# Kernel optimization log

Measured on AMD Instinct MI355X. Metric: run time of the kernel, lower is better.

Reference implementation:

```python
import jax, jax.numpy as jnp
import numpy as np

N, E, ND, D = 100000, 200000, 128, 32


def linear_bn(x, W, g, b, eps=1e-5):
    # Linear (no bias) followed by BatchNorm1d in training mode (batch stats)
    y = x @ W
    mu = jnp.mean(y, axis=0)
    var = jnp.var(y, axis=0)
    return g * (y - mu) * jax.lax.rsqrt(var + eps) + b


def setup_inputs() -> dict:
    key = jax.random.key(0)
    ks = jax.random.split(key, 16)
    s = 0.05
    return {
        "node": jax.random.normal(ks[0], (N, ND), jnp.float32),
        "edge_index": jax.random.randint(ks[1], (E, 2), 0, N, jnp.int64),
        "edge": jax.random.normal(ks[2], (E, D), jnp.float32),
        "hidden": jax.random.normal(ks[3], (1, E, D), jnp.float32),
        "W1": jax.random.normal(ks[4], (2 * ND, 256), jnp.float32) * s,
        "g1": jnp.ones((256,), jnp.float32), "b1": jnp.zeros((256,), jnp.float32),
        "W2": jax.random.normal(ks[5], (256, 256), jnp.float32) * s,
        "g2": jnp.ones((256,), jnp.float32), "b2": jnp.zeros((256,), jnp.float32),
        "W3": jax.random.normal(ks[6], (256, 128), jnp.float32) * s,
        "g3": jnp.ones((128,), jnp.float32), "b3": jnp.zeros((128,), jnp.float32),
        "W4": jax.random.normal(ks[7], (128, D * D), jnp.float32) * s,
        "g4": jnp.ones((D * D,), jnp.float32), "b4": jnp.zeros((D * D,), jnp.float32),
        "bias": jax.random.uniform(ks[8], (D,), jnp.float32, -1.0 / np.sqrt(D), 1.0 / np.sqrt(D)),
        "W_ih": jax.random.normal(ks[9], (3 * D, D), jnp.float32) * s,
        "W_hh": jax.random.normal(ks[10], (3 * D, D), jnp.float32) * s,
        "b_ih": jnp.zeros((3 * D,), jnp.float32),
        "b_hh": jnp.zeros((3 * D,), jnp.float32),
    }


def reference(node, edge_index, edge, hidden, W1, g1, b1, W2, g2, b2, W3, g3, b3,
              W4, g4, b4, bias, W_ih, W_hh, b_ih, b_hh):
    num_edge, edge_dim = edge.shape
    # gather endpoint node features and concat -> [E, 2*node_dim]
    x_ij = jnp.concatenate([node[edge_index[:, 0]], node[edge_index[:, 1]]], axis=1)
    h = jax.nn.relu(linear_bn(x_ij, W1, g1, b1))
    h = jax.nn.relu(linear_bn(h, W2, g2, b2))
    h = jax.nn.relu(linear_bn(h, W3, g3, b3))
    A = linear_bn(h, W4, g4, b4).reshape(num_edge, edge_dim, edge_dim)
    # per-edge small matmul: [E,1,D] @ [E,D,D] -> [E,D]
    message = jnp.einsum('ed,edf->ef', edge, A)
    message = jax.nn.relu(message + bias)
    # single-step GRU (seq_len=1, edges as batch)
    h0 = hidden[0]
    gi = message @ W_ih.T + b_ih
    gh = h0 @ W_hh.T + b_hh
    i_r, i_z, i_n = jnp.split(gi, 3, axis=1)
    h_r, h_z, h_n = jnp.split(gh, 3, axis=1)
    r = jax.nn.sigmoid(i_r + h_r)
    z = jax.nn.sigmoid(i_z + h_z)
    n = jnp.tanh(i_n + r * h_n)
    h_new = (1.0 - z) * n + z * h0
    return h_new, h_new[None]
```

## Files before the change

kernel.cpp:

```cpp
#include <hip/hip_runtime.h>
#include <hip/hip_fp16.h>

#define NE 200000
#define NT 6250
#define NT64 3125
#define GRAM_BLOCKS 512

__device__ float g_st[21248];
__device__ unsigned short g_c4h[1024];
__device__ int g_flag64;

#define SUM1 (&g_st[0])
#define SQ1  (&g_st[256])
#define SUM2 (&g_st[512])
#define SQ2  (&g_st[768])
#define SUM3 (&g_st[1024])
#define SQ3  (&g_st[1152])
#define GMAT (&g_st[1280])
#define CS3  (&g_st[17664])
#define A1   (&g_st[17792])
#define C1   (&g_st[18048])
#define A2   (&g_st[18304])
#define C2   (&g_st[18560])
#define A3   (&g_st[18816])
#define C3   (&g_st[18944])
#define A4   (&g_st[19072])
#define C4   (&g_st[20096])

typedef unsigned short u16;
typedef _Float16 f16x8 __attribute__((ext_vector_type(8)));
typedef float f32x4 __attribute__((ext_vector_type(4)));

__device__ __forceinline__ f32x4 mfma16(f16x8 a, f16x8 b, f32x4 c) {
  return __builtin_amdgcn_mfma_f32_16x16x32_f16(a, b, c, 0, 0, 0);
}
__device__ __forceinline__ u16 f2h(float x) {
  __half h = __float2half_rn(x);
  return *reinterpret_cast<u16*>(&h);
}
__device__ __forceinline__ float h2f(u16 s) {
  __half h = *reinterpret_cast<__half*>(&s);
  return __half2float(h);
}
__device__ __forceinline__ float relu_np(float t) { return (t < 0.f) ? 0.f : t; }
__device__ __forceinline__ unsigned packh2(float a, float b) {
  return (unsigned)f2h(a) | ((unsigned)f2h(b) << 16);
}

__global__ void GraphConv2_16518444221042_kernel(float* __restrict__ out,
                                                 float v, int n) {
  int i = blockIdx.x * 256 + threadIdx.x;
  if (i < n) out[i] = v;
}

__global__ void k_init(const int* __restrict__ e) {
  int i = blockIdx.x * 256 + threadIdx.x;
  if (i < 17792) g_st[i] = 0.f;
  if (i == 0) {
    int allz = 1;
    for (int k = 1; k < 128; k += 2) allz &= (e[k] == 0);
    g_flag64 = allz;
  }
}

__global__ void k_packA(const float* __restrict__ W1,
                        const float* __restrict__ W2,
                        const float* __restrict__ W3,
                        u16* __restrict__ dst) {
  int i = blockIdx.x * 256 + threadIdx.x;
  if (i >= 163840) return;
  float v;
  if (i < 65536) {
    int n = i >> 8, k = i & 255;
    v = W1[k * 256 + n];
  } else if (i < 131072) {
    int i2 = i - 65536, n = i2 >> 8, k = i2 & 255;
    v = W2[k * 256 + n];
  } else {
    int i2 = i - 131072, n = i2 >> 8, k = i2 & 255;
    v = W3[k * 128 + n];
  }
  dst[i] = f2h(v);
}

__global__ void k_packB(const float* __restrict__ W4,
                        const float* __restrict__ Wih,
                        const float* __restrict__ Whh,
                        u16* __restrict__ dst) {
  int i = blockIdx.x * 256 + threadIdx.x;
  if (i >= 137216) return;
  float v;
  if (i < 131072) {
    int n = i >> 7, k = i & 127;
    v = W4[(size_t)k * 1024 + n];
  } else if (i < 134144) {
    v = Wih[i - 131072];
  } else {
    v = Whh[i - 134144];
  }
  dst[i] = f2h(v);
}

__global__ void k_finalize(const float* __restrict__ g,
                           const float* __restrict__ b, int which, int C) {
  int j = threadIdx.x;
  if (j < C) {
    const float* sum = (which == 1) ? SUM1 : (which == 2) ? SUM2 : SUM3;
    const float* sq  = (which == 1) ? SQ1 : (which == 2) ? SQ2 : SQ3;
    float* aa = (which == 1) ? A1 : (which == 2) ? A2 : A3;
    float* cc = (which == 1) ? C1 : (which == 2) ? C2 : C3;
    const float invE = 1.f / (float)NE;
    float mu = sum[j] * invE;
    float var = fmaf(-mu, mu, sq[j] * invE);
    float s = rsqrtf(var + 1e-5f);
    float av = g[j] * s;
    aa[j] = av;
    cc[j] = fmaf(-av, mu, b[j]);
  }
}

__global__ __launch_bounds__(64) void k_finalize4(
    const float* __restrict__ W4, const float* __restrict__ g4,
    const float* __restrict__ b4) {
  __shared__ float wsh[128];
  const int lane = threadIdx.x;
  const float invE = 1.f / (float)NE;
  for (int j = blockIdx.x; j < 1024; j += gridDim.x) {
    float w0 = W4[lane * 1024 + j];
    float w1 = W4[(lane + 64) * 1024 + j];
    wsh[lane] = w0;
    wsh[lane + 64] = w1;
    __syncthreads();
    float s0 = 0.f, s1 = 0.f;
#pragma unroll 8
    for (int k = 0; k < 128; ++k) {
      float wk = wsh[k];
      s0 = fmaf(GMAT[lane * 128 + k], wk, s0);
      s1 = fmaf(GMAT[(lane + 64) * 128 + k], wk, s1);
    }
    float acc = w0 * s0 + w1 * s1;
    float mac = CS3[lane] * w0 + CS3[lane + 64] * w1;
#pragma unroll
    for (int off = 32; off > 0; off >>= 1) {
      acc += __shfl_down(acc, off);
      mac += __shfl_down(mac, off);
    }
    if (lane == 0) {
      float mu = mac * invE;
      float var = fmaf(-mu, mu, acc * invE);
      float s = rsqrtf(var + 1e-5f);
      float av = g4[j] * s;
      A4[j] = av;
      float cv = fmaf(-av, mu, b4[j]);
      C4[j] = cv;
      g_c4h[(j & 31) * 32 + (j >> 5)] = f2h(cv);
    }
    __syncthreads();
  }
}

template <int L>
__global__ __launch_bounds__(512) void k_gemmP(
    const float* __restrict__ node, const int* __restrict__ eidx,
    const u16* __restrict__ Yin, const u16* __restrict__ Wt,
    u16* __restrict__ Yout) {
  constexpr int CN = (L == 3) ? 128 : 256;
  constexpr int CTW = CN / 128;
  constexpr int LDH = 264;
  __shared__ __align__(16) u16 H[64 * LDH];
  __shared__ float csum_s[CN], csq_s[CN];
  __shared__ int idx_s[128];
  const int tid = threadIdx.x;
  float* SUMo = (L == 1) ? SUM1 : (L == 2) ? SUM2 : SUM3;
  float* SQo  = (L == 1) ? SQ1 : (L == 2) ? SQ2 : SQ3;
  const float* Ain = (L == 2) ? A1 : A2;
  const float* Cin = (L == 2) ? C1 : C2;

  const int l = tid & 63, w = tid >> 6;
  const int lr = l & 15, lg = l >> 4;

  f16x8 bfr[CTW][8];
#pragma unroll
  for (int c = 0; c < CTW; ++c)
#pragma unroll
    for (int kb = 0; kb < 8; ++kb)
      bfr[c][kb] = *(const f16x8*)&Wt[(size_t)((w * CTW + c) * 16 + lr) * 256 +
                                      kb * 32 + lg * 8];

  if (tid < CN) { csum_s[tid] = 0.f; csq_s[tid] = 0.f; }
  float sreg[CTW] = {}, qreg[CTW] = {};

  for (int t = blockIdx.x; t < NT64; t += gridDim.x) {
    const int r0 = t * 64;
    __syncthreads();
    if constexpr (L == 1) {
      if (tid < 128) {
        const int is64 = g_flag64;
        int m = tid & 63, sel = tid >> 6;
        int j = (r0 + m) * 2 + sel;
        int v = is64 ? eidx[j * 2] : eidx[j];
        v = v < 0 ? 0 : (v > 99999 ? 99999 : v);
        idx_s[sel * 64 + m] = v;
      }
      __syncthreads();
#pragma unroll
      for (int i = 0; i < 8; ++i) {
        int idx = tid + i * 512;
        int row = idx >> 6, col = (idx & 63) * 4;
        int sel = col >> 7, kc = col & 127;
        float4 v =
            *(const float4*)&node[(size_t)idx_s[sel * 64 + row] * 128 + kc];
        uint2 pk;
        pk.x = packh2(v.x, v.y);
        pk.y = packh2(v.z, v.w);
        *(uint2*)&H[row * LDH + col] = pk;
      }
    } else {
#pragma unroll
      for (int i = 0; i < 4; ++i) {
        int idx = tid + i * 512;
        int row = idx >> 5, col = (idx & 31) * 8;
        uint4 ld = *(const uint4*)&Yin[(size_t)(r0 + row) * 256 + col];
        const u16* sp = (const u16*)&ld;
        uint4 o;
        unsigned po[4];
#pragma unroll
        for (int p = 0; p < 4; ++p) {
          float v0 = relu_np(fmaf(Ain[col + 2 * p], h2f(sp[2 * p]),
                                  Cin[col + 2 * p]));
          float v1 = relu_np(fmaf(Ain[col + 2 * p + 1], h2f(sp[2 * p + 1]),
                                  Cin[col + 2 * p + 1]));
          po[p] = packh2(v0, v1);
        }
        o.x = po[0]; o.y = po[1]; o.z = po[2]; o.w = po[3];
        *(uint4*)&H[row * LDH + col] = o;
      }
    }
    __syncthreads();

    f32x4 acc[4][CTW] = {};
#pragma unroll
    for (int kb = 0; kb < 8; ++kb) {
      f16x8 a[4];
#pragma unroll
      for (int rt = 0; rt < 4; ++rt)
        a[rt] = *(const f16x8*)&H[(rt * 16 + lr) * LDH + kb * 32 + lg * 8];
#pragma unroll
      for (int c = 0; c < CTW; ++c)
#pragma unroll
        for (int rt = 0; rt < 4; ++rt)
          acc[rt][c] = mfma16(a[rt], bfr[c][kb], acc[rt][c]);
    }

#pragma unroll
    for (int c = 0; c < CTW; ++c) {
      const int col = (w * CTW + c) * 16 + lr;
#pragma unroll
      for (int rt = 0; rt < 4; ++rt)
#pragma unroll
        for (int r = 0; r < 4; ++r) {
          float v = acc[rt][c][r];
          sreg[c] += v;
          qreg[c] = fmaf(v, v, qreg[c]);
          int row = rt * 16 + lg * 4 + r;
          Yout[(size_t)(r0 + row) * CN + col] = f2h(v);
        }
    }
  }

  __syncthreads();
#pragma unroll
  for (int c = 0; c < CTW; ++c) {
    const int col = (w * CTW + c) * 16 + lr;
    atomicAdd(&csum_s[col], sreg[c]);
    atomicAdd(&csq_s[col], qreg[c]);
  }
  __syncthreads();
  if (tid < CN) {
    atomicAdd(&SUMo[tid], csum_s[tid]);
    atomicAdd(&SQo[tid], csq_s[tid]);
  }
}

__global__ __launch_bounds__(256, 2) void k_gram_m(const u16* __restrict__ y3g,
                                                   float* __restrict__ pg) {
  __shared__ u16 h3T[128 * 40];
  __shared__ float cred[128];
  const int tid = threadIdx.x;
  const int l = tid & 63, w = tid >> 6;
  const int lr = l & 15, lg = l >> 4;
  const int c4 = (tid & 31) * 4;
  const int rb = tid >> 5;
  f32x4 acc[2][8] = {};
  float csc[4] = {0.f, 0.f, 0.f, 0.f};

  for (int t = blockIdx.x; t < NT; t += gridDim.x) {
    const size_t r0 = (size_t)t * 32;
    __syncthreads();
#pragma unroll
    for (int i = 0; i < 4; ++i) {
      int row = rb + i * 8;
      ushort4 v = *(const ushort4*)&y3g[(r0 + row) * 128 + c4];
      float h[4];
      h[0] = relu_np(fmaf(A3[c4 + 0], h2f(v.x), C3[c4 + 0]));
      h[1] = relu_np(fmaf(A3[c4 + 1], h2f(v.y), C3[c4 + 1]));
      h[2] = relu_np(fmaf(A3[c4 + 2], h2f(v.z), C3[c4 + 2]));
      h[3] = relu_np(fmaf(A3[c4 + 3], h2f(v.w), C3[c4 + 3]));
#pragma unroll
      for (int j = 0; j < 4; ++j) {
        csc[j] += h[j];
        int col = c4 + j;
        int swz = ((col >> 2) & 3) << 3;
        h3T[col * 40 + (row ^ swz)] = f2h(h[j]);
      }
    }
    __syncthreads();
    f16x8 bfr[8];
#pragma unroll
    for (int tj = 0; tj < 8; ++tj) {
      int col = tj * 16 + lr;
      int swz = ((col >> 2) & 3) << 3;
      bfr[tj] = *(const f16x8*)&h3T[col * 40 + ((lg * 8) ^ swz)];
    }
#pragma unroll
    for (int ri = 0; ri < 2; ++ri) {
      f16x8 a = bfr[w * 2 + ri];
#pragma unroll
      for (int tj = 0; tj < 8; ++tj)
        acc[ri][tj] = mfma16(a, bfr[tj], acc[ri][tj]);
    }
  }
  float* my = pg + (size_t)blockIdx.x * 16384;
#pragma unroll
  for (int ri = 0; ri < 2; ++ri)
#pragma unroll
    for (int tj = 0; tj < 8; ++tj)
#pragma unroll
      for (int r = 0; r < 4; ++r) {
        int row = (w * 2 + ri) * 16 + lg * 4 + r, col = tj * 16 + lr;
        my[row * 128 + col] = acc[ri][tj][r];
      }
  if (tid < 128) cred[tid] = 0.f;
  __syncthreads();
#pragma unroll
  for (int j = 0; j < 4; ++j) atomicAdd(&cred[c4 + j], csc[j]);
  __syncthreads();
  if (tid < 128) atomicAdd(&CS3[tid], cred[tid]);
}

__global__ void k_gramred(const float* __restrict__ pg) {
  int g = blockIdx.x * 256 + threadIdx.x;
  float s = 0.f;
  for (int p = 0; p < GRAM_BLOCKS; ++p) s += pg[(size_t)p * 16384 + g];
  GMAT[g] = s;
}

__global__ __launch_bounds__(256, 2) void k_final128(
    const u16* __restrict__ y3g, const u16* __restrict__ w4t,
    const u16* __restrict__ wihh, const u16* __restrict__ whhh,
    const float* __restrict__ edge, const float* __restrict__ hidden,
    const float* __restrict__ bias, const float* __restrict__ bih,
    const float* __restrict__ bhh, float* __restrict__ out) {
  __shared__ __align__(16) u16 H3[128 * 136];
  __shared__ u16 SLAB[32 * 136];
  __shared__ u16 EDS[128 * 40];
  __shared__ u16 MSG[128 * 40];
  __shared__ u16 H0S[128 * 40];
  float* OUTBUF = (float*)H3;
  const int tid = threadIdx.x;
  const size_t r0 = (size_t)blockIdx.x * 128;

#pragma unroll
  for (int i = 0; i < 16; ++i) {
    int idx = tid + i * 256;
    int row = idx >> 5, col = (idx & 31) * 4;
    size_t sr = r0 + row;
    if (sr >= NE) sr = NE - 1;
    ushort4 v = *(const ushort4*)&y3g[sr * 128 + col];
    float h0 = relu_np(fmaf(A3[col + 0], h2f(v.x), C3[col + 0]));
    float h1 = relu_np(fmaf(A3[col + 1], h2f(v.y), C3[col + 1]));
    float h2v = relu_np(fmaf(A3[col + 2], h2f(v.z), C3[col + 2]));
    float h3v = relu_np(fmaf(A3[col + 3], h2f(v.w), C3[col + 3]));
    uint2 pk;
    pk.x = packh2(h0, h1);
    pk.y = packh2(h2v, h3v);
    *(uint2*)&H3[row * 136 + col] = pk;
  }
#pragma unroll
  for (int i = 0; i < 4; ++i) {
    int idx = tid + i * 256;
    int row = idx >> 3, col = (idx & 7) * 4;
    size_t sr = r0 + row;
    if (sr >= NE) sr = NE - 1;
    float4 ev = *(const float4*)&edge[sr * 32 + col];
    uint2 pe;
    pe.x = packh2(ev.x, ev.y);
    pe.y = packh2(ev.z, ev.w);
    *(uint2*)&EDS[row * 40 + col] = pe;
    float4 hv = *(const float4*)&hidden[sr * 32 + col];
    uint2 ph;
    ph.x = packh2(hv.x, hv.y);
    ph.y = packh2(hv.z, hv.w);
    *(uint2*)&H0S[row * 40 + col] = ph;
  }
  __syncthreads();

  const int l = tid & 63, w = tid >> 6;
  const int lr = l & 15, lg = l >> 4;
  f16x8 af[2][4];
#pragma unroll
  for (int rt = 0; rt < 2; ++rt)
#pragma unroll
    for (int kb = 0; kb < 4; ++kb)
      af[rt][kb] =
          *(const f16x8*)&H3[((w * 2 + rt) * 16 + lr) * 136 + kb * 32 + lg * 8];

  float mp[2][4][2] = {};
  for (int cg = 0; cg < 32; ++cg) {
    __syncthreads();
    {
      int c = tid >> 3, ch = tid & 7;
#pragma unroll
      for (int q = 0; q < 2; ++q) {
        int kk = (ch + q * 8) * 8;
        *(uint4*)&SLAB[c * 136 + kk] =
            *(const uint4*)&w4t[(size_t)(cg * 32 + c) * 128 + kk];
      }
    }
    __syncthreads();
#pragma unroll
    for (int ci = 0; ci < 2; ++ci) {
      f16x8 b[4];
#pragma unroll
      for (int kb = 0; kb < 4; ++kb)
        b[kb] = *(const f16x8*)&SLAB[(ci * 16 + lr) * 136 + kb * 32 + lg * 8];
      const float a4v = A4[cg * 32 + ci * 16 + lr];
#pragma unroll
      for (int rt = 0; rt < 2; ++rt) {
        f32x4 acc = {0.f, 0.f, 0.f, 0.f};
#pragma unroll
        for (int kb = 0; kb < 4; ++kb) acc = mfma16(af[rt][kb], b[kb], acc);
#pragma unroll
        for (int r = 0; r < 4; ++r) {
          int e = (w * 2 + rt) * 16 + lg * 4 + r;
          float ed = h2f(EDS[e * 40 + cg]);
          mp[rt][r][ci] = fmaf(ed * a4v, acc[r], mp[rt][r][ci]);
        }
      }
    }
  }

  f32x4 m0[2][2];
#pragma unroll
  for (int rt = 0; rt < 2; ++rt) {
    f16x8 ae = *(const f16x8*)&EDS[((w * 2 + rt) * 16 + lr) * 40 + lg * 8];
#pragma unroll
    for (int ci = 0; ci < 2; ++ci) {
      f16x8 bc = *(const f16x8*)&g_c4h[(ci * 16 + lr) * 32 + lg * 8];
      f32x4 z = {0.f, 0.f, 0.f, 0.f};
      m0[rt][ci] = mfma16(ae, bc, z);
    }
  }
#pragma unroll
  for (int rt = 0; rt < 2; ++rt)
#pragma unroll
    for (int ci = 0; ci < 2; ++ci)
#pragma unroll
      for (int r = 0; r < 4; ++r) {
        int e = (w * 2 + rt) * 16 + lg * 4 + r;
        int f = ci * 16 + lr;
        float v = relu_np(mp[rt][r][ci] + m0[rt][ci][r] + bias[f]);
        MSG[e * 40 + f] = f2h(v);
      }
  __syncthreads();

  f32x4 gi[2][6], gh[2][6];
#pragma unroll
  for (int rt = 0; rt < 2; ++rt) {
    f16x8 am = *(const f16x8*)&MSG[((w * 2 + rt) * 16 + lr) * 40 + lg * 8];
    f16x8 ah = *(const f16x8*)&H0S[((w * 2 + rt) * 16 + lr) * 40 + lg * 8];
#pragma unroll
    for (int ct = 0; ct < 6; ++ct) {
      f16x8 bi = *(const f16x8*)&wihh[(ct * 16 + lr) * 32 + lg * 8];
      f16x8 bh = *(const f16x8*)&whhh[(ct * 16 + lr) * 32 + lg * 8];
      f32x4 z = {0.f, 0.f, 0.f, 0.f};
      gi[rt][ct] = mfma16(am, bi, z);
      gh[rt][ct] = mfma16(ah, bh, z);
    }
  }
#pragma unroll
  for (int rt = 0; rt < 2; ++rt)
#pragma unroll
    for (int r = 0; r < 4; ++r) {
      int e = (w * 2 + rt) * 16 + lg * 4 + r;
#pragma unroll
      for (int hf = 0; hf < 2; ++hf) {
        int f = hf * 16 + lr;
        float xr = gi[rt][hf][r] + bih[f];
        float xz = gi[rt][2 + hf][r] + bih[32 + f];
        float xn = gi[rt][4 + hf][r] + bih[64 + f];
        float hr = gh[rt][hf][r] + bhh[f];
        float hz = gh[rt][2 + hf][r] + bhh[32 + f];
        float hn = gh[rt][4 + hf][r] + bhh[64 + f];
        float rg = 1.f / (1.f + __expf(-(xr + hr)));
        float zg = 1.f / (1.f + __expf(-(xz + hz)));
        float ng = tanhf(fmaf(rg, hn, xn));
        float h0v = h2f(H0S[e * 40 + f]);
        if (r0 + e < NE) h0v = hidden[(r0 + e) * 32 + f];
        OUTBUF[e * 32 + f] = fmaf(zg, h0v - ng, ng);
      }
    }
  __syncthreads();
#pragma unroll
  for (int i = 0; i < 4; ++i) {
    int off = tid * 4 + i * 1024;
    size_t g = r0 * 32 + off;
    if (g < (size_t)NE * 32) {
      float4 v = *(const float4*)&OUTBUF[off];
      *(float4*)&out[g] = v;
      *(float4*)&out[(size_t)NE * 32 + g] = v;
    }
  }
}

extern "C" void kernel_launch(void* const* d_in, const int* in_sizes, int n_in,
                              void* d_out, int out_size, void* d_ws,
                              size_t ws_size, hipStream_t stream) {
  float* out = (float*)d_out;

  static const int EXP[21] = {
      12800000, 400000, 6400000, 6400000,
      65536, 256, 256, 65536, 256, 256, 32768, 128, 128,
      131072, 1024, 1024, 32, 3072, 3072, 96, 96};
  int bad = -1;
  if (n_in != 21) bad = 25;
  else
    for (int i = 0; i < 21; ++i)
      if (in_sizes[i] != EXP[i]) { bad = i; break; }
  if (bad < 0 && out_size != 12800000) bad = 22;
  const size_t Y1B = (size_t)NE * 256 * 2;
  if (bad < 0 && (!d_ws || ws_size < 2 * Y1B)) bad = 24;
  if (bad >= 0) {
    float code = 3.0e7f + (float)bad * 1.0e6f;
    GraphConv2_16518444221042_kernel<<<(out_size + 255) / 256, 256, 0, stream>>>(
        out, code, out_size);
    return;
  }

  const float* node   = (const float*)d_in[0];
  const int*   eidx   = (const int*)d_in[1];
  const float* edge   = (const float*)d_in[2];
  const float* hidden = (const float*)d_in[3];
  const float* W1 = (const float*)d_in[4];
  const float* g1 = (const float*)d_in[5];
  const float* b1 = (const float*)d_in[6];
  const float* W2 = (const float*)d_in[7];
  const float* g2 = (const float*)d_in[8];
  const float* b2 = (const float*)d_in[9];
  const float* W3 = (const float*)d_in[10];
  const float* g3 = (const float*)d_in[11];
  const float* b3 = (const float*)d_in[12];
  const float* W4 = (const float*)d_in[13];
  const float* g4 = (const float*)d_in[14];
  const float* b4 = (const float*)d_in[15];
  const float* bias = (const float*)d_in[16];
  const float* Wih = (const float*)d_in[17];
  const float* Whh = (const float*)d_in[18];
  const float* bih = (const float*)d_in[19];
  const float* bhh = (const float*)d_in[20];

  u16* y1 = (u16*)d_ws;
  u16* y2 = (u16*)d_ws + (size_t)NE * 256;
  u16* y3 = (u16*)d_ws;

  u16* pkA = (u16*)d_out;
  u16* w1t = pkA;
  u16* w2t = pkA + 65536;
  u16* w3t = pkA + 131072;
  u16* w4t  = y2;
  u16* wihh = y2 + 131072;
  u16* whhh = y2 + 134144;
  float* pgram = (float*)(y2 + 2097152);

  k_init<<<70, 256, 0, stream>>>(eidx);
  k_packA<<<640, 256, 0, stream>>>(W1, W2, W3, pkA);

  k_gemmP<1><<<512, 512, 0, stream>>>(node, eidx, nullptr, w1t, y1);
  k_finalize<<<1, 256, 0, stream>>>(g1, b1, 1, 256);
  k_gemmP<2><<<512, 512, 0, stream>>>(nullptr, nullptr, y1, w2t, y2);
  k_finalize<<<1, 256, 0, stream>>>(g2, b2, 2, 256);
  k_gemmP<3><<<512, 512, 0, stream>>>(nullptr, nullptr, y2, w3t, y3);
  k_finalize<<<1, 256, 0, stream>>>(g3, b3, 3, 128);
  k_packB<<<537, 256, 0, stream>>>(W4, Wih, Whh, y2);
  k_gram_m<<<GRAM_BLOCKS, 256, 0, stream>>>(y3, pgram);
  k_gramred<<<64, 256, 0, stream>>>(pgram);
  k_finalize4<<<128, 64, 0, stream>>>(W4, g4, b4);
  k_final128<<<1563, 256, 0, stream>>>(y3, w4t, wihh, whhh, edge, hidden,
                                       bias, bih, bhh, out);
}
```

Baseline: 453.3 us.

## Shrink final kernel tile to 64 edges per block for higher occupancy

```diff
diff --git a/kernel.cpp b/kernel.cpp
--- a/kernel.cpp
+++ b/kernel.cpp
@@ -355,28 +355,25 @@
   GMAT[g] = s;
 }
 
-__global__ __launch_bounds__(256, 2) void k_final128(
+__global__ __launch_bounds__(256, 4) void k_final64(
     const u16* __restrict__ y3g, const u16* __restrict__ w4t,
     const u16* __restrict__ wihh, const u16* __restrict__ whhh,
     const float* __restrict__ edge, const float* __restrict__ hidden,
     const float* __restrict__ bias, const float* __restrict__ bih,
     const float* __restrict__ bhh, float* __restrict__ out) {
-  __shared__ __align__(16) u16 H3[128 * 136];
-  __shared__ u16 SLAB[32 * 136];
-  __shared__ u16 EDS[128 * 40];
-  __shared__ u16 MSG[128 * 40];
-  __shared__ u16 H0S[128 * 40];
+  __shared__ __align__(16) u16 H3[64 * 136];
+  __shared__ __align__(16) u16 SLAB[32 * 136];
+  __shared__ __align__(16) u16 EDS[64 * 40];
   float* OUTBUF = (float*)H3;
+  u16* MSGu = H3 + 4096;
   const int tid = threadIdx.x;
-  const size_t r0 = (size_t)blockIdx.x * 128;
-
-#pragma unroll
-  for (int i = 0; i < 16; ++i) {
+  const size_t r0 = (size_t)blockIdx.x * 64;
+
+#pragma unroll
+  for (int i = 0; i < 8; ++i) {
     int idx = tid + i * 256;
     int row = idx >> 5, col = (idx & 31) * 4;
-    size_t sr = r0 + row;
-    if (sr >= NE) sr = NE - 1;
-    ushort4 v = *(const ushort4*)&y3g[sr * 128 + col];
+    ushort4 v = *(const ushort4*)&y3g[(r0 + row) * 128 + col];
     float h0 = relu_np(fmaf(A3[col + 0], h2f(v.x), C3[col + 0]));
     float h1 = relu_np(fmaf(A3[col + 1], h2f(v.y), C3[col + 1]));
     float h2v = relu_np(fmaf(A3[col + 2], h2f(v.z), C3[col + 2]));
@@ -387,35 +384,25 @@
     *(uint2*)&H3[row * 136 + col] = pk;
   }
 #pragma unroll
-  for (int i = 0; i < 4; ++i) {
+  for (int i = 0; i < 2; ++i) {
     int idx = tid + i * 256;
     int row = idx >> 3, col = (idx & 7) * 4;
-    size_t sr = r0 + row;
-    if (sr >= NE) sr = NE - 1;
-    float4 ev = *(const float4*)&edge[sr * 32 + col];
+    float4 ev = *(const float4*)&edge[(r0 + row) * 32 + col];
     uint2 pe;
     pe.x = packh2(ev.x, ev.y);
     pe.y = packh2(ev.z, ev.w);
     *(uint2*)&EDS[row * 40 + col] = pe;
-    float4 hv = *(const float4*)&hidden[sr * 32 + col];
-    uint2 ph;
-    ph.x = packh2(hv.x, hv.y);
-    ph.y = packh2(hv.z, hv.w);
-    *(uint2*)&H0S[row * 40 + col] = ph;
   }
   __syncthreads();
 
   const int l = tid & 63, w = tid >> 6;
   const int lr = l & 15, lg = l >> 4;
-  f16x8 af[2][4];
-#pragma unroll
-  for (int rt = 0; rt < 2; ++rt)
-#pragma unroll
-    for (int kb = 0; kb < 4; ++kb)
-      af[rt][kb] =
-          *(const f16x8*)&H3[((w * 2 + rt) * 16 + lr) * 136 + kb * 32 + lg * 8];
-
-  float mp[2][4][2] = {};
+  f16x8 af[4];
+#pragma unroll
+  for (int kb = 0; kb < 4; ++kb)
+    af[kb] = *(const f16x8*)&H3[(w * 16 + lr) * 136 + kb * 32 + lg * 8];
+
+  float mp[4][2] = {};
   for (int cg = 0; cg < 32; ++cg) {
     __syncthreads();
     {
@@ -435,91 +422,88 @@
       for (int kb = 0; kb < 4; ++kb)
         b[kb] = *(const f16x8*)&SLAB[(ci * 16 + lr) * 136 + kb * 32 + lg * 8];
       const float a4v = A4[cg * 32 + ci * 16 + lr];
-#pragma unroll
-      for (int rt = 0; rt < 2; ++rt) {
-        f32x4 acc = {0.f, 0.f, 0.f, 0.f};
-#pragma unroll
-        for (int kb = 0; kb < 4; ++kb) acc = mfma16(af[rt][kb], b[kb], acc);
-#pragma unroll
-        for (int r = 0; r < 4; ++r) {
-          int e = (w * 2 + rt) * 16 + lg * 4 + r;
-          float ed = h2f(EDS[e * 40 + cg]);
-          mp[rt][r][ci] = fmaf(ed * a4v, acc[r], mp[rt][r][ci]);
-        }
-      }
-    }
-  }
-
-  f32x4 m0[2][2];
-#pragma unroll
-  for (int rt = 0; rt < 2; ++rt) {
-    f16x8 ae = *(const f16x8*)&EDS[((w * 2 + rt) * 16 + lr) * 40 + lg * 8];
+      f32x4 acc = {0.f, 0.f, 0.f, 0.f};
+#pragma unroll
+      for (int kb = 0; kb < 4; ++kb) acc = mfma16(af[kb], b[kb], acc);
+#pragma unroll
+      for (int r = 0; r < 4; ++r) {
+        int e = w * 16 + lg * 4 + r;
+        float ed = h2f(EDS[e * 40 + cg]);
+        mp[r][ci] = fmaf(ed * a4v, acc[r], mp[r][ci]);
+      }
+    }
+  }
+
+  f32x4 m0[2];
+  {
+    f16x8 ae = *(const f16x8*)&EDS[(w * 16 + lr) * 40 + lg * 8];
 #pragma unroll
     for (int ci = 0; ci < 2; ++ci) {
       f16x8 bc = *(const f16x8*)&g_c4h[(ci * 16 + lr) * 32 + lg * 8];
       f32x4 z = {0.f, 0.f, 0.f, 0.f};
-      m0[rt][ci] = mfma16(ae, bc, z);
-    }
-  }
-#pragma unroll
-  for (int rt = 0; rt < 2; ++rt)
-#pragma unroll
-    for (int ci = 0; ci < 2; ++ci)
-#pragma unroll
-      for (int r = 0; r < 4; ++r) {
-        int e = (w * 2 + rt) * 16 + lg * 4 + r;
-        int f = ci * 16 + lr;
-        float v = relu_np(mp[rt][r][ci] + m0[rt][ci][r] + bias[f]);
-        MSG[e * 40 + f] = f2h(v);
-      }
-  __syncthreads();
-
-  f32x4 gi[2][6], gh[2][6];
-#pragma unroll
-  for (int rt = 0; rt < 2; ++rt) {
-    f16x8 am = *(const f16x8*)&MSG[((w * 2 + rt) * 16 + lr) * 40 + lg * 8];
-    f16x8 ah = *(const f16x8*)&H0S[((w * 2 + rt) * 16 + lr) * 40 + lg * 8];
-#pragma unroll
-    for (int ct = 0; ct < 6; ++ct) {
-      f16x8 bi = *(const f16x8*)&wihh[(ct * 16 + lr) * 32 + lg * 8];
-      f16x8 bh = *(const f16x8*)&whhh[(ct * 16 + lr) * 32 + lg * 8];
-      f32x4 z = {0.f, 0.f, 0.f, 0.f};
-      gi[rt][ct] = mfma16(am, bi, z);
-      gh[rt][ct] = mfma16(ah, bh, z);
-    }
-  }
-#pragma unroll
-  for (int rt = 0; rt < 2; ++rt)
+      m0[ci] = mfma16(ae, bc, z);
+    }
+  }
+#pragma unroll
+  for (int ci = 0; ci < 2; ++ci)
 #pragma unroll
     for (int r = 0; r < 4; ++r) {
-      int e = (w * 2 + rt) * 16 + lg * 4 + r;
-#pragma unroll
-      for (int hf = 0; hf < 2; ++hf) {
-        int f = hf * 16 + lr;
-        float xr = gi[rt][hf][r] + bih[f];
-        float xz = gi[rt][2 + hf][r] + bih[32 + f];
-        float xn = gi[rt][4 + hf][r] + bih[64 + f];
-        float hr = gh[rt][hf][r] + bhh[f];
-        float hz = gh[rt][2 + hf][r] + bhh[32 + f];
-        float hn = gh[rt][4 + hf][r] + bhh[64 + f];
-        float rg = 1.f / (1.f + __expf(-(xr + hr)));
-        float zg = 1.f / (1.f + __expf(-(xz + hz)));
-        float ng = tanhf(fmaf(rg, hn, xn));
-        float h0v = h2f(H0S[e * 40 + f]);
-        if (r0 + e < NE) h0v = hidden[(r0 + e) * 32 + f];
-        OUTBUF[e * 32 + f] = fmaf(zg, h0v - ng, ng);
-      }
-    }
-  __syncthreads();
-#pragma unroll
-  for (int i = 0; i < 4; ++i) {
+      int e = w * 16 + lg * 4 + r;
+      int f = ci * 16 + lr;
+      float v = relu_np(mp[r][ci] + m0[ci][r] + bias[f]);
+      MSGu[e * 40 + f] = f2h(v);
+    }
+  __syncthreads();
+
+  f16x8 am = *(const f16x8*)&MSGu[(w * 16 + lr) * 40 + lg * 8];
+  f16x8 ah;
+  {
+    int e = w * 16 + lr;
+    float4 h0a = *(const float4*)&hidden[(r0 + e) * 32 + lg * 8];
+    float4 h0b = *(const float4*)&hidden[(r0 + e) * 32 + lg * 8 + 4];
+    union { unsigned u[4]; f16x8 h; } uu;
+    uu.u[0] = packh2(h0a.x, h0a.y);
+    uu.u[1] = packh2(h0a.z, h0a.w);
+    uu.u[2] = packh2(h0b.x, h0b.y);
+    uu.u[3] = packh2(h0b.z, h0b.w);
+    ah = uu.h;
+  }
+  f32x4 gi[6], gh[6];
+#pragma unroll
+  for (int ct = 0; ct < 6; ++ct) {
+    f16x8 bi = *(const f16x8*)&wihh[(ct * 16 + lr) * 32 + lg * 8];
+    f16x8 bh = *(const f16x8*)&whhh[(ct * 16 + lr) * 32 + lg * 8];
+    f32x4 z = {0.f, 0.f, 0.f, 0.f};
+    gi[ct] = mfma16(am, bi, z);
+    gh[ct] = mfma16(ah, bh, z);
+  }
+#pragma unroll
+  for (int r = 0; r < 4; ++r) {
+    int e = w * 16 + lg * 4 + r;
+#pragma unroll
+    for (int hf = 0; hf < 2; ++hf) {
+      int f = hf * 16 + lr;
+      float xr = gi[hf][r] + bih[f];
+      float xz = gi[2 + hf][r] + bih[32 + f];
+      float xn = gi[4 + hf][r] + bih[64 + f];
+      float hr = gh[hf][r] + bhh[f];
+      float hz = gh[2 + hf][r] + bhh[32 + f];
+      float hn = gh[4 + hf][r] + bhh[64 + f];
+      float rg = 1.f / (1.f + __expf(-(xr + hr)));
+      float zg = 1.f / (1.f + __expf(-(xz + hz)));
+      float ng = tanhf(fmaf(rg, hn, xn));
+      float h0v = hidden[(r0 + e) * 32 + f];
+      OUTBUF[e * 32 + f] = fmaf(zg, h0v - ng, ng);
+    }
+  }
+  __syncthreads();
+#pragma unroll
+  for (int i = 0; i < 2; ++i) {
     int off = tid * 4 + i * 1024;
     size_t g = r0 * 32 + off;
-    if (g < (size_t)NE * 32) {
-      float4 v = *(const float4*)&OUTBUF[off];
-      *(float4*)&out[g] = v;
-      *(float4*)&out[(size_t)NE * 32 + g] = v;
-    }
+    float4 v = *(const float4*)&OUTBUF[off];
+    *(float4*)&out[g] = v;
+    *(float4*)&out[(size_t)NE * 32 + g] = v;
   }
 }
 
@@ -595,6 +579,6 @@
   k_gram_m<<<GRAM_BLOCKS, 256, 0, stream>>>(y3, pgram);
   k_gramred<<<64, 256, 0, stream>>>(pgram);
   k_finalize4<<<128, 64, 0, stream>>>(W4, g4, b4);
-  k_final128<<<1563, 256, 0, stream>>>(y3, w4t, wihh, whhh, edge, hidden,
-                                       bias, bih, bhh, out);
-}
+  k_final64<<<NT64, 256, 0, stream>>>(y3, w4t, wihh, whhh, edge, hidden,
+                                      bias, bih, bhh, out);
+}
```

Result: faster. 429.4 us (-5.3%).
